# Kernel optimization log

Hardware: AMD Instinct MI355X
Metric: run time of the kernel (lower is better)

The kernel has to match this reference:

```python
import jax, jax.numpy as jnp
import numpy as np

N_NODES = 20000
N_EDGES = 320000
N_FEAT = 128
N_CLASS = 10
NEG_SLOPE = 0.2  # PyG GATConv default LeakyReLU slope


def gat_conv(x, src, dst, ew, W, a_src, a_dst, b, heads, ch, concat):
    """PyG-style GATConv with multiplicative edge_weight on messages.
    x: [N, Fin]; src/dst: [E] (self-loops already included); ew: [E].
    """
    N = x.shape[0]
    h = (x @ W).reshape(N, heads, ch)                      # [N,H,C]
    al_s = jnp.sum(h * a_src, axis=-1)                     # [N,H]
    al_d = jnp.sum(h * a_dst, axis=-1)                     # [N,H]
    e = jax.nn.leaky_relu(al_s[src] + al_d[dst], NEG_SLOPE)  # [E,H]
    # segment softmax over incoming edges of each target node
    m = jax.ops.segment_max(e, dst, num_segments=N)        # [N,H]
    ex = jnp.exp(e - m[dst])
    den = jax.ops.segment_sum(ex, dst, num_segments=N)     # [N,H]
    alpha = ex / (den[dst] + 1e-16)                        # [E,H]
    msg = h[src] * (alpha * ew[:, None])[..., None]        # [E,H,C]
    out = jax.ops.segment_sum(msg, dst, num_segments=N)    # [N,H,C]
    out = out.reshape(N, heads * ch) if concat else out.mean(axis=1)
    return out + b


def setup_inputs() -> dict:
    key = jax.random.key(0)
    ks = jax.random.split(key, 20)
    d = {}
    d["x"] = jax.random.normal(ks[0], (N_NODES, N_FEAT), dtype=jnp.float32)
    d["edge_index"] = jax.random.randint(ks[1], (2, N_EDGES), 0, N_NODES, dtype=jnp.int32)
    d["edge_weight"] = jnp.ones((N_EDGES,), dtype=jnp.float32)

    def glorot(k, shape):
        fan = shape[0] + shape[-1]
        return jax.random.uniform(k, shape, jnp.float32, -1.0, 1.0) * np.sqrt(6.0 / fan)

    H1, C1 = 4, 256
    H3, C3 = 6, N_CLASS
    d["W1"] = glorot(ks[2], (N_FEAT, H1 * C1))
    d["a1s"] = glorot(ks[3], (H1, C1)) * 0.1
    d["a1d"] = glorot(ks[4], (H1, C1)) * 0.1
    d["b1"] = jnp.zeros((H1 * C1,), jnp.float32)
    d["lw1"] = glorot(ks[5], (N_FEAT, H1 * C1))
    d["lb1"] = jnp.zeros((H1 * C1,), jnp.float32)

    d["W2"] = glorot(ks[6], (H1 * C1, H1 * C1))
    d["a2s"] = glorot(ks[7], (H1, C1)) * 0.1
    d["a2d"] = glorot(ks[8], (H1, C1)) * 0.1
    d["b2"] = jnp.zeros((H1 * C1,), jnp.float32)
    d["lw2"] = glorot(ks[9], (H1 * C1, H1 * C1))
    d["lb2"] = jnp.zeros((H1 * C1,), jnp.float32)

    d["W3"] = glorot(ks[10], (H1 * C1, H3 * C3))
    d["a3s"] = glorot(ks[11], (H3, C3)) * 0.1
    d["a3d"] = glorot(ks[12], (H3, C3)) * 0.1
    d["b3"] = jnp.zeros((C3,), jnp.float32)
    d["lw3"] = glorot(ks[13], (H1 * C1, C3))
    d["lb3"] = jnp.zeros((C3,), jnp.float32)
    return d


def reference(x, edge_index, edge_weight,
              W1, a1s, a1d, b1, lw1, lb1,
              W2, a2s, a2d, b2, lw2, lb2,
              W3, a3s, a3d, b3, lw3, lb3):
    N = x.shape[0]
    # PyG GATConv adds self-loops (fill edge_weight with 1.0)
    loop = jnp.arange(N, dtype=edge_index.dtype)
    src = jnp.concatenate([edge_index[0], loop])
    dst = jnp.concatenate([edge_index[1], loop])
    ew = jnp.concatenate([edge_weight, jnp.ones((N,), edge_weight.dtype)])

    h = jax.nn.elu(gat_conv(x, src, dst, ew, W1, a1s, a1d, b1, 4, 256, True)
                   + (x @ lw1 + lb1))
    h = jax.nn.elu(gat_conv(h, src, dst, ew, W2, a2s, a2d, b2, 4, 256, True)
                   + (h @ lw2 + lb2))
    out = gat_conv(h, src, dst, ew, W3, a3s, a3d, b3, 6, N_CLASS, False) \
          + (h @ lw3 + lb3)
    return out
```

## Files before the change

### kernel.cpp

```cpp
#include <hip/hip_runtime.h>

typedef __attribute__((ext_vector_type(8))) short s16x8;
typedef __attribute__((ext_vector_type(8))) __bf16 bf16x8;
typedef __attribute__((ext_vector_type(4))) float f32x4;

__device__ inline float bf2f(ushort u){ return __uint_as_float(((unsigned)u)<<16); }
__device__ inline ushort f2bf(float f){
  unsigned u = __float_as_uint(f);
  unsigned r = (u + 0x7fffu + ((u>>16)&1u)) >> 16;
  return (ushort)r;
}

__device__ inline void gl_lds16(const ushort* g, ushort* l){
  __builtin_amdgcn_global_load_lds(
      (const __attribute__((address_space(1))) unsigned int*)g,
      (__attribute__((address_space(3))) unsigned int*)l,
      16, 0, 0);
}

__global__ void k_count(const int* __restrict__ ei, int* __restrict__ counts,
                        int E, int ET){
  int e = blockIdx.x*256 + threadIdx.x;
  if (e >= ET) return;
  int dst = (e < E) ? ei[E + e] : (e - E);
  atomicAdd(&counts[dst], 1);
}

__global__ __launch_bounds__(1024) void k_scan(const int* __restrict__ cnt,
                                               int* __restrict__ indptr, int N){
  __shared__ int part[1024];
  int t = threadIdx.x;
  int per = (N + 1023) / 1024;
  int base = t * per;
  int s = 0;
  for (int i = 0; i < per; ++i){ int idx = base + i; if (idx < N) s += cnt[idx]; }
  part[t] = s; __syncthreads();
  for (int off = 1; off < 1024; off <<= 1){
    int v = (t >= off) ? part[t-off] : 0;
    __syncthreads();
    if (t >= off) part[t] += v;
    __syncthreads();
  }
  int run = (t == 0) ? 0 : part[t-1];
  for (int i = 0; i < per; ++i){
    int idx = base + i;
    if (idx < N){ indptr[idx] = run; run += cnt[idx]; }
  }
  if (t == 1023) indptr[N] = run;
}

__global__ void k_fill(const int* __restrict__ ei, const float* __restrict__ ew,
                       const int* __restrict__ indptr, int* __restrict__ cursor,
                       int* __restrict__ csrc, float* __restrict__ cew,
                       int E, int ET){
  int e = blockIdx.x*256 + threadIdx.x;
  if (e >= ET) return;
  int src, dst; float w;
  if (e < E){ src = ei[e]; dst = ei[E + e]; w = ew[e]; }
  else { src = dst = e - E; w = 1.0f; }
  int pos = indptr[dst] + atomicAdd(&cursor[dst], 1);
  csrc[pos] = src; cew[pos] = w;
}

__global__ void k_f2b(const float* __restrict__ x, ushort* __restrict__ xb, int n){
  int i = blockIdx.x*256 + threadIdx.x;
  if (i < n) xb[i] = f2bf(x[i]);
}

__global__ __launch_bounds__(256) void k_packB(
    const float* __restrict__ W, const float* __restrict__ LW,
    ushort* __restrict__ BT, int K, int NW, int NL, int Npad)
{
  __shared__ float tile[32][33];
  int k0 = blockIdx.x*32, n0 = blockIdx.y*32;
  int c = threadIdx.x & 31, r4 = threadIdx.x >> 5;
  #pragma unroll
  for (int rr = 0; rr < 32; rr += 8){
    int k = k0 + r4 + rr, n = n0 + c;
    float v = 0.f;
    if (k < K){
      if (n < NW)            v = W[(size_t)k*NW + n];
      else if (n < NW + NL)  v = LW[(size_t)k*NL + (n - NW)];
    }
    tile[r4+rr][c] = v;
  }
  __syncthreads();
  #pragma unroll
  for (int rr = 0; rr < 32; rr += 8){
    int n = n0 + r4 + rr, k = k0 + c;
    if (n < Npad && k < K) BT[(size_t)n*K + k] = f2bf(tile[c][r4+rr]);
  }
}

__global__ __launch_bounds__(256) void k_gemm(
    const ushort* __restrict__ A, const ushort* __restrict__ BT,
    ushort* __restrict__ Gatt, ushort* __restrict__ Skip,
    int K, int GW, int SW, int NCB, int CPX)
{
  __shared__ ushort As[128*64];
  __shared__ ushort Bs[128*64];
  const int bid = blockIdx.x;
  const int lb = CPX ? ((bid & 7)*CPX + (bid >> 3)) : bid;
  const size_t row0 = (size_t)(lb / NCB) * 128;
  const size_t col0 = (size_t)(lb % NCB) * 128;
  const int t = threadIdx.x;
  const int l = t & 63, w = t >> 6;
  const int wr = w >> 1, wc = w & 1;
  const int sr = l >> 3;
  const int sk = ((l & 7) ^ sr) << 3;
  const ushort* gA = A  + (row0 + w*8 + sr)*(size_t)K + sk;
  const ushort* gB = BT + (col0 + w*8 + sr)*(size_t)K + sk;
  ushort* lA = As + w*512;
  ushort* lB = Bs + w*512;
  const int rf = l & 15;
  const int g4 = l >> 4;
  f32x4 acc[4][4] = {};

  for (int k0 = 0; k0 < K; k0 += 64){
    #pragma unroll
    for (int i = 0; i < 4; ++i){
      gl_lds16(gA + k0 + (size_t)(i*32)*K, lA + i*2048);
      gl_lds16(gB + k0 + (size_t)(i*32)*K, lB + i*2048);
    }
    __syncthreads();
    #pragma unroll
    for (int kk = 0; kk < 2; ++kk){
      const int koff = ((((kk<<2) | g4) ^ (rf & 7)) << 3);
      bf16x8 af[4], bfr[4];
      #pragma unroll
      for (int i = 0; i < 4; ++i)
        af[i] = __builtin_bit_cast(bf16x8, *(const s16x8*)(As + (wr*64 + i*16 + rf)*64 + koff));
      #pragma unroll
      for (int j = 0; j < 4; ++j)
        bfr[j] = __builtin_bit_cast(bf16x8, *(const s16x8*)(Bs + (wc*64 + j*16 + rf)*64 + koff));
      #pragma unroll
      for (int i = 0; i < 4; ++i)
        #pragma unroll
        for (int j = 0; j < 4; ++j)
          acc[i][j] = __builtin_amdgcn_mfma_f32_16x16x32_bf16(af[i], bfr[j], acc[i][j], 0, 0, 0);
    }
    __syncthreads();
  }

  #pragma unroll
  for (int i = 0; i < 4; ++i){
    #pragma unroll
    for (int j = 0; j < 4; ++j){
      int gc = (int)col0 + wc*64 + j*16 + rf;
      #pragma unroll
      for (int r = 0; r < 4; ++r){
        size_t gr = row0 + wr*64 + i*16 + (g4<<2) + r;
        float v = acc[i][j][r];
        if (gc < GW)            Gatt[gr*GW + gc] = f2bf(v);
        else if (gc < GW + SW)  Skip[gr*SW + (gc - GW)] = f2bf(v);
      }
    }
  }
}

__global__ __launch_bounds__(256) void k_al(const ushort* __restrict__ Gatt,
    const float* __restrict__ a_s, const float* __restrict__ a_d,
    float* __restrict__ als, float* __restrict__ ald, int N){
  int gw = (blockIdx.x*blockDim.x + threadIdx.x) >> 6;
  int l = threadIdx.x & 63;
  if (gw >= N) return;
  const ushort* row = Gatt + (size_t)gw*1024;
  int c0 = l*16;
  float ps = 0.f, pd = 0.f;
  #pragma unroll
  for (int i = 0; i < 16; i += 4){
    ushort4 v = *(const ushort4*)(row + c0 + i);
    float f0 = bf2f(v.x), f1 = bf2f(v.y), f2 = bf2f(v.z), f3 = bf2f(v.w);
    ps += f0*a_s[c0+i] + f1*a_s[c0+i+1] + f2*a_s[c0+i+2] + f3*a_s[c0+i+3];
    pd += f0*a_d[c0+i] + f1*a_d[c0+i+1] + f2*a_d[c0+i+2] + f3*a_d[c0+i+3];
  }
  #pragma unroll
  for (int off = 8; off; off >>= 1){
    ps += __shfl_down(ps, off);
    pd += __shfl_down(pd, off);
  }
  if ((l & 15) == 0){
    als[(size_t)gw*4 + (l>>4)] = ps;
    ald[(size_t)gw*4 + (l>>4)] = pd;
  }
}

__global__ __launch_bounds__(256) void k_agg(
    const ushort* __restrict__ Gatt,
    const ushort* __restrict__ Skip,
    const float*  __restrict__ als,
    const float*  __restrict__ ald,
    const float*  __restrict__ bias,
    const float*  __restrict__ lbias,
    const int*    __restrict__ indptr,
    const int*    __restrict__ csrc,
    const float*  __restrict__ cew,
    ushort* __restrict__ Hout,
    int N)
{
  const int n = blockIdx.x;
  const int t = threadIdx.x;
  const int l = t & 63, w = t >> 6;
  const int beg = indptr[n];
  const int deg = indptr[n+1] - beg;
  __shared__ float s_ald[4], s_m[4], s_den[4];
  __shared__ int   s_src[64];
  __shared__ float s_w[64][4];
  __shared__ float s_part[3][64][16];
  if (t < 4) s_ald[t] = ald[(size_t)n*4 + t];
  __syncthreads();
  const float aldh = s_ald[w];
  float mx = -1e30f;
  for (int i = l; i < deg; i += 64){
    int s = csrc[beg+i];
    float e = als[(size_t)s*4 + w] + aldh;
    e = e > 0.f ? e : 0.2f*e;
    mx = fmaxf(mx, e);
  }
  #pragma unroll
  for (int off = 32; off; off >>= 1) mx = fmaxf(mx, __shfl_xor(mx, off));
  if (l == 0) s_m[w] = mx;
  __syncthreads();
  const float mh = s_m[w];
  float den = 0.f;
  for (int i = l; i < deg; i += 64){
    int s = csrc[beg+i];
    float e = als[(size_t)s*4 + w] + aldh;
    e = e > 0.f ? e : 0.2f*e;
    den += __expf(e - mh);
  }
  #pragma unroll
  for (int off = 32; off; off >>= 1) den += __shfl_xor(den, off);
  if (l == 0) s_den[w] = den + 1e-16f;
  __syncthreads();
  const int h2 = l >> 4;
  float a[16];
  #pragma unroll
  for (int q = 0; q < 16; ++q) a[q] = 0.f;
  for (int c0 = 0; c0 < deg; c0 += 64){
    int nc = min(64, deg - c0);
    int ei2 = t >> 2, hh = t & 3;
    if (ei2 < nc){
      int s = csrc[beg + c0 + ei2];
      if (hh == 0) s_src[ei2] = s;
      float e = als[(size_t)s*4 + hh] + s_ald[hh];
      e = e > 0.f ? e : 0.2f*e;
      s_w[ei2][hh] = __expf(e - s_m[hh]) / s_den[hh] * cew[beg + c0 + ei2];
    }
    __syncthreads();
    for (int j = w; j < nc; j += 4){
      int s = s_src[j];
      float wg = s_w[j][h2];
      const ushort* rp = Gatt + (size_t)s*1024 + l*16;
      s16x8 h0 = *(const s16x8*)rp;
      s16x8 h1 = *(const s16x8*)(rp + 8);
      #pragma unroll
      for (int q = 0; q < 8; ++q) a[q] += wg * bf2f((ushort)h0[q]);
      #pragma unroll
      for (int q = 0; q < 8; ++q) a[q+8] += wg * bf2f((ushort)h1[q]);
    }
    __syncthreads();
  }
  if (w){
    #pragma unroll
    for (int q = 0; q < 16; ++q) s_part[w-1][l][q] = a[q];
  }
  __syncthreads();
  if (w == 0){
    #pragma unroll
    for (int q = 0; q < 16; ++q) a[q] += s_part[0][l][q] + s_part[1][l][q] + s_part[2][l][q];
    const int col = l*16;
    s16x8 sk0 = *(const s16x8*)(Skip + (size_t)n*1024 + col);
    s16x8 sk1 = *(const s16x8*)(Skip + (size_t)n*1024 + col + 8);
    s16x8 ov0, ov1;
    #pragma unroll
    for (int q = 0; q < 8; ++q){
      float v = a[q] + bias[col+q] + lbias[col+q] + bf2f((ushort)sk0[q]);
      v = v > 0.f ? v : __expf(v) - 1.f;
      ov0[q] = (short)f2bf(v);
      float v2 = a[q+8] + bias[col+8+q] + lbias[col+8+q] + bf2f((ushort)sk1[q]);
      v2 = v2 > 0.f ? v2 : __expf(v2) - 1.f;
      ov1[q] = (short)f2bf(v2);
    }
    *(s16x8*)(Hout + (size_t)n*1024 + col)     = ov0;
    *(s16x8*)(Hout + (size_t)n*1024 + col + 8) = ov1;
  }
}

__global__ void k_al3(const ushort* __restrict__ G3, const float* __restrict__ a_s,
                      const float* __restrict__ a_d,
                      float* __restrict__ als, float* __restrict__ ald, int N){
  int n = blockIdx.x*256 + threadIdx.x;
  if (n >= N) return;
  const ushort* row = G3 + (size_t)n*60;
  #pragma unroll
  for (int h = 0; h < 6; ++h){
    float ps = 0.f, pd = 0.f;
    #pragma unroll
    for (int c = 0; c < 10; ++c){
      float v = bf2f(row[h*10 + c]);
      ps += v * a_s[h*10 + c];
      pd += v * a_d[h*10 + c];
    }
    als[(size_t)n*6 + h] = ps;
    ald[(size_t)n*6 + h] = pd;
  }
}

__global__ __launch_bounds__(64) void k_agg3(
    const ushort* __restrict__ G3,
    const ushort* __restrict__ Skip3,
    const float*  __restrict__ als,
    const float*  __restrict__ ald,
    const float*  __restrict__ b3,
    const float*  __restrict__ lb3,
    const int*    __restrict__ indptr,
    const int*    __restrict__ csrc,
    const float*  __restrict__ cew,
    float* __restrict__ out, int N)
{
  const int n = blockIdx.x;
  const int l = threadIdx.x;
  const int beg = indptr[n], deg = indptr[n+1] - beg;
  __shared__ float s_aldh[6];
  __shared__ int   s_src[64];
  __shared__ float s_wgt[64][6];
  __shared__ float s_o[6][10];
  if (l < 6) s_aldh[l] = ald[(size_t)n*6 + l];
  __syncthreads();
  float m0=-1e30f,m1=-1e30f,m2=-1e30f,m3=-1e30f,m4=-1e30f,m5=-1e30f;
  float d0=0.f,d1=0.f,d2=0.f,d3=0.f,d4=0.f,d5=0.f;
  for (int c0 = 0; c0 < deg; c0 += 64){
    int nc = min(64, deg - c0);
    bool act = l < nc;
    int s = act ? csrc[beg + c0 + l] : 0;
#define HP(hh, mm, dd) { \
    float e = -1e30f; \
    if (act){ float r_ = als[(size_t)s*6 + hh] + s_aldh[hh]; e = r_ > 0.f ? r_ : 0.2f*r_; } \
    float cm = e; \
    for (int o_ = 32; o_; o_ >>= 1) cm = fmaxf(cm, __shfl_xor(cm, o_)); \
    float nm = fmaxf(mm, cm); \
    float ex = act ? __expf(e - nm) : 0.f; \
    for (int o_ = 32; o_; o_ >>= 1) ex += __shfl_xor(ex, o_); \
    dd = dd * __expf(mm - nm) + ex; mm = nm; }
    HP(0,m0,d0) HP(1,m1,d1) HP(2,m2,d2) HP(3,m3,d3) HP(4,m4,d4) HP(5,m5,d5)
#undef HP
  }
  const int h = l / 10, c = l % 10;
  float o = 0.f;
  for (int c0 = 0; c0 < deg; c0 += 64){
    int nc = min(64, deg - c0);
    if (l < nc){
      int s = csrc[beg + c0 + l];
      s_src[l] = s;
      float w_ = cew[beg + c0 + l];
#define WP(hh, mm, dd) { \
      float r_ = als[(size_t)s*6 + hh] + s_aldh[hh]; \
      float e = r_ > 0.f ? r_ : 0.2f*r_; \
      s_wgt[l][hh] = __expf(e - mm) / (dd + 1e-16f) * w_; }
      WP(0,m0,d0) WP(1,m1,d1) WP(2,m2,d2) WP(3,m3,d3) WP(4,m4,d4) WP(5,m5,d5)
#undef WP
    }
    __syncthreads();
    if (l < 60){
      for (int i = 0; i < nc; ++i)
        o += s_wgt[i][h] * bf2f(G3[(size_t)s_src[i]*60 + l]);
    }
    __syncthreads();
  }
  if (l < 60) s_o[h][c] = o;
  __syncthreads();
  if (l < 10){
    float v = (s_o[0][l]+s_o[1][l]+s_o[2][l]+s_o[3][l]+s_o[4][l]+s_o[5][l]) * (1.0f/6.0f);
    v += b3[l] + lb3[l] + bf2f(Skip3[(size_t)n*10 + l]);
    out[(size_t)n*10 + l] = v;
  }
}

extern "C" void kernel_launch(void* const* d_in, const int* in_sizes, int n_in,
                              void* d_out, int out_size, void* d_ws, size_t ws_size,
                              hipStream_t stream)
{
  const int N = 20000, F = 128, E = 320000, ET = E + N;
  const int Mpad = 20096;
  const int F1 = 1024, NT = 2048;
  const int NWG = (Mpad/128)*(NT/128);

  const float* x   = (const float*)d_in[0];
  const int*   ei  = (const int*)  d_in[1];
  const float* ew  = (const float*)d_in[2];
  const float* W1  = (const float*)d_in[3];
  const float* a1s = (const float*)d_in[4];
  const float* a1d = (const float*)d_in[5];
  const float* b1  = (const float*)d_in[6];
  const float* lw1 = (const float*)d_in[7];
  const float* lb1 = (const float*)d_in[8];
  const float* W2  = (const float*)d_in[9];
  const float* a2s = (const float*)d_in[10];
  const float* a2d = (const float*)d_in[11];
  const float* b2  = (const float*)d_in[12];
  const float* lw2 = (const float*)d_in[13];
  const float* lb2 = (const float*)d_in[14];
  const float* W3  = (const float*)d_in[15];
  const float* a3s = (const float*)d_in[16];
  const float* a3d = (const float*)d_in[17];
  const float* b3  = (const float*)d_in[18];
  const float* lw3 = (const float*)d_in[19];
  const float* lb3 = (const float*)d_in[20];

  char* ws = (char*)d_ws;
  size_t off = 0;
  auto alloc = [&](size_t bytes) -> void* {
    void* p = ws + off;
    off = (off + bytes + 255) & ~(size_t)255;
    return p;
  };
  ushort* Gatt = (ushort*)alloc((size_t)Mpad*F1*2);
  ushort* Skip = (ushort*)alloc((size_t)Mpad*F1*2);
  ushort* H    = (ushort*)alloc((size_t)Mpad*F1*2);
  ushort* xb   = (ushort*)alloc((size_t)Mpad*F*2);
  ushort* BT   = (ushort*)alloc((size_t)NT*1024*2);
  float*  als  = (float*) alloc((size_t)N*6*4);
  float*  ald  = (float*) alloc((size_t)N*6*4);
  int*    counts = (int*)alloc((size_t)N*4);
  int*    cursor = (int*)alloc((size_t)N*4);
  int*    indptr = (int*)alloc((size_t)(N+1)*4);
  int*    csrc   = (int*)alloc((size_t)ET*4);
  float*  cew    = (float*)alloc((size_t)ET*4);
  if (off > ws_size) return;

  hipMemsetAsync(counts, 0, (size_t)N*4, stream);
  hipMemsetAsync(cursor, 0, (size_t)N*4, stream);
  hipMemsetAsync(xb + (size_t)N*F,  0, (size_t)(Mpad-N)*F*2,  stream);
  hipMemsetAsync(H  + (size_t)N*F1, 0, (size_t)(Mpad-N)*F1*2, stream);

  k_count<<<(ET+255)/256, 256, 0, stream>>>(ei, counts, E, ET);
  k_scan<<<1, 1024, 0, stream>>>(counts, indptr, N);
  k_fill<<<(ET+255)/256, 256, 0, stream>>>(ei, ew, indptr, cursor, csrc, cew, E, ET);
  k_f2b<<<(N*F+255)/256, 256, 0, stream>>>(x, xb, N*F);

  k_packB<<<dim3((F+31)/32, NT/32), 256, 0, stream>>>(W1, lw1, BT, F, 1024, 1024, NT);
  k_gemm<<<dim3(NWG), 256, 0, stream>>>(xb, BT, Gatt, Skip, F, 1024, 1024, NT/128, NWG/8);
  k_al<<<(N+3)/4, 256, 0, stream>>>(Gatt, a1s, a1d, als, ald, N);
  k_agg<<<N, 256, 0, stream>>>(Gatt, Skip, als, ald, b1, lb1, indptr, csrc, cew, H, N);

  k_packB<<<dim3(F1/32, NT/32), 256, 0, stream>>>(W2, lw2, BT, F1, 1024, 1024, NT);
  k_gemm<<<dim3(NWG), 256, 0, stream>>>(H, BT, Gatt, Skip, F1, 1024, 1024, NT/128, NWG/8);
  k_al<<<(N+3)/4, 256, 0, stream>>>(Gatt, a2s, a2d, als, ald, N);
  k_agg<<<N, 256, 0, stream>>>(Gatt, Skip, als, ald, b2, lb2, indptr, csrc, cew, H, N);

  k_packB<<<dim3(F1/32, 128/32), 256, 0, stream>>>(W3, lw3, BT, F1, 60, 10, 128);
  k_gemm<<<dim3(Mpad/128), 256, 0, stream>>>(H, BT, Gatt, Skip, F1, 60, 10, 1, 0);
  k_al3<<<(N+255)/256, 256, 0, stream>>>(Gatt, a3s, a3d, als, ald, N);
  k_agg3<<<N, 64, 0, stream>>>(Gatt, Skip, als, ald, b3, lb3, indptr, csrc, cew,
                               (float*)d_out, N);
}
```

Measured before the change: 510.2 us.

## Single-pass softmax for low-degree nodes, vectorize conversions, fold padding memsets into kernels

Adds a fast path to the aggregation kernel for nodes with at most 64 incoming edges. It computes the edge logits once into shared memory and does the max and sum reductions with wave shuffles, instead of three passes that each re-gather als. The float-to-bf16 conversion and the attention-logit kernel now use 8-wide vector loads and stores. Zeroing of the padding rows moves into the f2b and agg kernels (agg now launches over Mpad blocks), and the two counter memsets merge into one. This removes memset launches and redundant gathers, at the cost of extra idle blocks for padding rows and more code-path divergence.

After: 501.3 us. No clear change (-1.7%).

```diff
diff --git a/kernel.cpp b/kernel.cpp
--- a/kernel.cpp
+++ b/kernel.cpp
@@ -62,9 +62,18 @@
   csrc[pos] = src; cew[pos] = w;
 }
 
-__global__ void k_f2b(const float* __restrict__ x, ushort* __restrict__ xb, int n){
+__global__ void k_f2b(const float* __restrict__ x, ushort* __restrict__ xb,
+                      int n8valid, int n8total){
   int i = blockIdx.x*256 + threadIdx.x;
-  if (i < n) xb[i] = f2bf(x[i]);
+  if (i >= n8total) return;
+  s16x8 o = {0,0,0,0,0,0,0,0};
+  if (i < n8valid){
+    const float4* p = (const float4*)x + (size_t)i*2;
+    float4 a = p[0], b = p[1];
+    o[0]=(short)f2bf(a.x); o[1]=(short)f2bf(a.y); o[2]=(short)f2bf(a.z); o[3]=(short)f2bf(a.w);
+    o[4]=(short)f2bf(b.x); o[5]=(short)f2bf(b.y); o[6]=(short)f2bf(b.z); o[7]=(short)f2bf(b.w);
+  }
+  *((s16x8*)xb + i) = o;
 }
 
 __global__ __launch_bounds__(256) void k_packB(
@@ -166,13 +175,14 @@
   if (gw >= N) return;
   const ushort* row = Gatt + (size_t)gw*1024;
   int c0 = l*16;
+  s16x8 v0 = *(const s16x8*)(row + c0);
+  s16x8 v1 = *(const s16x8*)(row + c0 + 8);
   float ps = 0.f, pd = 0.f;
   #pragma unroll
-  for (int i = 0; i < 16; i += 4){
-    ushort4 v = *(const ushort4*)(row + c0 + i);
-    float f0 = bf2f(v.x), f1 = bf2f(v.y), f2 = bf2f(v.z), f3 = bf2f(v.w);
-    ps += f0*a_s[c0+i] + f1*a_s[c0+i+1] + f2*a_s[c0+i+2] + f3*a_s[c0+i+3];
-    pd += f0*a_d[c0+i] + f1*a_d[c0+i+1] + f2*a_d[c0+i+2] + f3*a_d[c0+i+3];
+  for (int q = 0; q < 8; ++q){
+    float f0 = bf2f((ushort)v0[q]), f1 = bf2f((ushort)v1[q]);
+    ps += f0*a_s[c0+q] + f1*a_s[c0+8+q];
+    pd += f0*a_d[c0+q] + f1*a_d[c0+8+q];
   }
   #pragma unroll
   for (int off = 8; off; off >>= 1){
@@ -200,6 +210,11 @@
 {
   const int n = blockIdx.x;
   const int t = threadIdx.x;
+  if (n >= N){
+    ushort4 z = {0,0,0,0};
+    *(ushort4*)(Hout + (size_t)n*1024 + t*4) = z;
+    return;
+  }
   const int l = t & 63, w = t >> 6;
   const int beg = indptr[n];
   const int deg = indptr[n+1] - beg;
@@ -209,49 +224,77 @@
   __shared__ float s_part[3][64][16];
   if (t < 4) s_ald[t] = ald[(size_t)n*4 + t];
   __syncthreads();
-  const float aldh = s_ald[w];
-  float mx = -1e30f;
-  for (int i = l; i < deg; i += 64){
-    int s = csrc[beg+i];
-    float e = als[(size_t)s*4 + w] + aldh;
-    e = e > 0.f ? e : 0.2f*e;
-    mx = fmaxf(mx, e);
-  }
-  #pragma unroll
-  for (int off = 32; off; off >>= 1) mx = fmaxf(mx, __shfl_xor(mx, off));
-  if (l == 0) s_m[w] = mx;
-  __syncthreads();
-  const float mh = s_m[w];
-  float den = 0.f;
-  for (int i = l; i < deg; i += 64){
-    int s = csrc[beg+i];
-    float e = als[(size_t)s*4 + w] + aldh;
-    e = e > 0.f ? e : 0.2f*e;
-    den += __expf(e - mh);
-  }
-  #pragma unroll
-  for (int off = 32; off; off >>= 1) den += __shfl_xor(den, off);
-  if (l == 0) s_den[w] = den + 1e-16f;
-  __syncthreads();
+  const bool fast = (deg <= 64);
+
+  if (fast){
+    int e2 = t >> 2, hh = t & 3;
+    if (e2 < deg){
+      int s = csrc[beg + e2];
+      if (hh == 0) s_src[e2] = s;
+      float r_ = als[(size_t)s*4 + hh] + s_ald[hh];
+      s_w[e2][hh] = r_ > 0.f ? r_ : 0.2f*r_;
+    }
+    __syncthreads();
+    float mye = (l < deg) ? s_w[l][w] : -1e30f;
+    float mx = mye;
+    #pragma unroll
+    for (int o = 32; o; o >>= 1) mx = fmaxf(mx, __shfl_xor(mx, o));
+    float ex = (l < deg) ? __expf(mye - mx) : 0.f;
+    float den = ex;
+    #pragma unroll
+    for (int o = 32; o; o >>= 1) den += __shfl_xor(den, o);
+    den += 1e-16f;
+    if (l < deg) s_w[l][w] = ex / den * cew[beg + l];
+    __syncthreads();
+  } else {
+    const float aldh = s_ald[w];
+    float mx = -1e30f;
+    for (int i = l; i < deg; i += 64){
+      int s = csrc[beg+i];
+      float e = als[(size_t)s*4 + w] + aldh;
+      e = e > 0.f ? e : 0.2f*e;
+      mx = fmaxf(mx, e);
+    }
+    #pragma unroll
+    for (int off = 32; off; off >>= 1) mx = fmaxf(mx, __shfl_xor(mx, off));
+    if (l == 0) s_m[w] = mx;
+    __syncthreads();
+    const float mh = s_m[w];
+    float den = 0.f;
+    for (int i = l; i < deg; i += 64){
+      int s = csrc[beg+i];
+      float e = als[(size_t)s*4 + w] + aldh;
+      e = e > 0.f ? e : 0.2f*e;
+      den += __expf(e - mh);
+    }
+    #pragma unroll
+    for (int off = 32; off; off >>= 1) den += __shfl_xor(den, off);
+    if (l == 0) s_den[w] = den + 1e-16f;
+    __syncthreads();
+  }
+
   const int h2 = l >> 4;
+  const ushort* gbase = Gatt + (size_t)l*16;
   float a[16];
   #pragma unroll
   for (int q = 0; q < 16; ++q) a[q] = 0.f;
   for (int c0 = 0; c0 < deg; c0 += 64){
     int nc = min(64, deg - c0);
-    int ei2 = t >> 2, hh = t & 3;
-    if (ei2 < nc){
-      int s = csrc[beg + c0 + ei2];
-      if (hh == 0) s_src[ei2] = s;
-      float e = als[(size_t)s*4 + hh] + s_ald[hh];
-      e = e > 0.f ? e : 0.2f*e;
-      s_w[ei2][hh] = __expf(e - s_m[hh]) / s_den[hh] * cew[beg + c0 + ei2];
-    }
-    __syncthreads();
+    if (!fast){
+      int ei2 = t >> 2, hh = t & 3;
+      if (ei2 < nc){
+        int s = csrc[beg + c0 + ei2];
+        if (hh == 0) s_src[ei2] = s;
+        float e = als[(size_t)s*4 + hh] + s_ald[hh];
+        e = e > 0.f ? e : 0.2f*e;
+        s_w[ei2][hh] = __expf(e - s_m[hh]) / s_den[hh] * cew[beg + c0 + ei2];
+      }
+      __syncthreads();
+    }
     for (int j = w; j < nc; j += 4){
       int s = s_src[j];
       float wg = s_w[j][h2];
-      const ushort* rp = Gatt + (size_t)s*1024 + l*16;
+      const ushort* rp = gbase + (size_t)s*1024;
       s16x8 h0 = *(const s16x8*)rp;
       s16x8 h1 = *(const s16x8*)(rp + 8);
       #pragma unroll
@@ -422,32 +465,28 @@
   ushort* BT   = (ushort*)alloc((size_t)NT*1024*2);
   float*  als  = (float*) alloc((size_t)N*6*4);
   float*  ald  = (float*) alloc((size_t)N*6*4);
-  int*    counts = (int*)alloc((size_t)N*4);
-  int*    cursor = (int*)alloc((size_t)N*4);
+  int*    counts = (int*)alloc((size_t)2*N*4);
+  int*    cursor = counts + N;
   int*    indptr = (int*)alloc((size_t)(N+1)*4);
   int*    csrc   = (int*)alloc((size_t)ET*4);
   float*  cew    = (float*)alloc((size_t)ET*4);
   if (off > ws_size) return;
 
-  hipMemsetAsync(counts, 0, (size_t)N*4, stream);
-  hipMemsetAsync(cursor, 0, (size_t)N*4, stream);
-  hipMemsetAsync(xb + (size_t)N*F,  0, (size_t)(Mpad-N)*F*2,  stream);
-  hipMemsetAsync(H  + (size_t)N*F1, 0, (size_t)(Mpad-N)*F1*2, stream);
-
+  hipMemsetAsync(counts, 0, (size_t)2*N*4, stream);
   k_count<<<(ET+255)/256, 256, 0, stream>>>(ei, counts, E, ET);
   k_scan<<<1, 1024, 0, stream>>>(counts, indptr, N);
   k_fill<<<(ET+255)/256, 256, 0, stream>>>(ei, ew, indptr, cursor, csrc, cew, E, ET);
-  k_f2b<<<(N*F+255)/256, 256, 0, stream>>>(x, xb, N*F);
+  k_f2b<<<(Mpad*F/8+255)/256, 256, 0, stream>>>(x, xb, N*F/8, Mpad*F/8);
 
   k_packB<<<dim3((F+31)/32, NT/32), 256, 0, stream>>>(W1, lw1, BT, F, 1024, 1024, NT);
   k_gemm<<<dim3(NWG), 256, 0, stream>>>(xb, BT, Gatt, Skip, F, 1024, 1024, NT/128, NWG/8);
   k_al<<<(N+3)/4, 256, 0, stream>>>(Gatt, a1s, a1d, als, ald, N);
-  k_agg<<<N, 256, 0, stream>>>(Gatt, Skip, als, ald, b1, lb1, indptr, csrc, cew, H, N);
+  k_agg<<<Mpad, 256, 0, stream>>>(Gatt, Skip, als, ald, b1, lb1, indptr, csrc, cew, H, N);
 
   k_packB<<<dim3(F1/32, NT/32), 256, 0, stream>>>(W2, lw2, BT, F1, 1024, 1024, NT);
   k_gemm<<<dim3(NWG), 256, 0, stream>>>(H, BT, Gatt, Skip, F1, 1024, 1024, NT/128, NWG/8);
   k_al<<<(N+3)/4, 256, 0, stream>>>(Gatt, a2s, a2d, als, ald, N);
-  k_agg<<<N, 256, 0, stream>>>(Gatt, Skip, als, ald, b2, lb2, indptr, csrc, cew, H, N);
+  k_agg<<<Mpad, 256, 0, stream>>>(Gatt, Skip, als, ald, b2, lb2, indptr, csrc, cew, H, N);
 
   k_packB<<<dim3(F1/32, 128/32), 256, 0, stream>>>(W3, lw3, BT, F1, 60, 10, 128);
   k_gemm<<<dim3(Mpad/128), 256, 0, stream>>>(H, BT, Gatt, Skip, F1, 60, 10, 1, 0);
```
